# Kernel optimization log

Measured on AMD Instinct MI355X. Metric: run time of the kernel, lower is better.

## Reference

```python
import math
import jax, jax.numpy as jnp
import numpy as np

D_MODEL = 1024
D_HIDDEN = 4096
N_EXPERTS = 8
TOP_K = 2
CAPACITY_FACTOR = 1.25


def setup_inputs() -> dict:
    key = jax.random.key(0)
    ks = jax.random.split(key, 8)
    s = 0.02
    x = jax.random.normal(ks[0], (4, 2048, D_MODEL), dtype=jnp.float32)
    router_w = jax.random.normal(ks[1], (D_MODEL, N_EXPERTS), dtype=jnp.float32) * s
    router_b = jnp.zeros((N_EXPERTS,), dtype=jnp.float32)
    w1 = jax.random.normal(ks[2], (N_EXPERTS, D_MODEL, D_HIDDEN), dtype=jnp.float32) * s
    b1 = jnp.zeros((N_EXPERTS, D_HIDDEN), dtype=jnp.float32)
    w2 = jax.random.normal(ks[3], (N_EXPERTS, D_HIDDEN, D_MODEL), dtype=jnp.float32) * s
    b2 = jnp.zeros((N_EXPERTS, D_MODEL), dtype=jnp.float32)
    return {"x": x, "router_w": router_w, "router_b": router_b,
            "w1": w1, "b1": b1, "w2": w2, "b2": b2}


def reference(x, router_w, router_b, w1, b1, w2, b2):
    B, T, D = x.shape
    N = B * T
    E = N_EXPERTS
    capacity = max(1, math.ceil(N / E * CAPACITY_FACTOR))

    x_flat = x.reshape(N, D)
    # Router (torch casts input to float32 for router)
    logits = x_flat.astype(jnp.float32) @ router_w + router_b          # [N, E]
    gates = jax.nn.softmax(logits, axis=-1)                            # [N, E]

    _, topk_idx = jax.lax.top_k(gates, TOP_K)                          # [N, k]
    expert_mask = jax.nn.one_hot(topk_idx, E, dtype=jnp.int32).sum(1)  # [N, E]

    # Capacity masking via cumulative position per expert
    pos = jnp.cumsum(expert_mask, axis=0) - 1                          # [N, E]
    expert_mask = expert_mask * (pos < capacity)
    valid = expert_mask > 0                                            # [N, E] bool

    # Dispatch: scatter tokens into [E, capacity, D] buffers (invalid -> slot `capacity`)
    pos_c = jnp.where(valid, pos, capacity)                            # [N, E]
    e_idx = jnp.broadcast_to(jnp.arange(E), (N, E))
    dispatched = (x_flat[:, None, :] * valid[:, :, None].astype(x.dtype))
    buf = jnp.zeros((E, capacity + 1, D), x.dtype).at[
        e_idx.ravel(), pos_c.ravel()].add(dispatched.reshape(N * E, D))
    buf = buf[:, :capacity]                                            # [E, C, D]

    # Per-expert FFN as batched GEMMs (GELU exact, matching nn.GELU default)
    h = jax.nn.gelu(jnp.einsum('ecd,edh->ech', buf, w1) + b1[:, None, :],
                    approximate=False)
    out = jnp.einsum('ech,ehd->ecd', h, w2) + b2[:, None, :]           # [E, C, D]

    # Combine: gather each token's expert outputs, weight by raw softmax gate
    pos_g = jnp.minimum(pos_c, capacity - 1)
    gathered = out[e_idx, pos_g]                                       # [N, E, D]
    weights = (gates * valid).astype(x.dtype)                          # [N, E]
    y = jnp.einsum('ned,ne->nd', gathered, weights)
    return y.reshape(B, T, D)
```

## Files before the change

### kernel.cpp

```cpp
#include <hip/hip_runtime.h>
#include <math.h>

#define D_MODEL 1024
#define D_HIDDEN 4096
#define NEXP 8
#define NTOK 8192
#define CAP 1280

#define BM 128
#define BN 128
#define BK2 64

typedef __attribute__((ext_vector_type(8))) short short8x;
typedef __attribute__((ext_vector_type(4))) short short4x;
typedef __attribute__((ext_vector_type(4))) float float4x;

__device__ __forceinline__ short f2bf(float f) {
  unsigned u = __float_as_uint(f);
  unsigned r = (u + 0x7FFFu + ((u >> 16) & 1u)) >> 16;
  return (short)r;
}
__device__ __forceinline__ float bf2f(short s) {
  return __uint_as_float(((unsigned)(unsigned short)s) << 16);
}
__device__ __forceinline__ float gelu_fast(float v) {
  float u2 = v * (1.5957691216f + 0.0713548163f * v * v);
  return v / (1.0f + __expf(-u2));
}

#define GLDS16(g, l)                                                        \
  __builtin_amdgcn_global_load_lds(                                         \
      (const __attribute__((address_space(1))) void*)(g),                   \
      (__attribute__((address_space(3))) void*)(l), 16, 0, 0)

__global__ __launch_bounds__(256) void convert_x_kernel(
    const float* __restrict__ x, short* __restrict__ xbf) {
  size_t i = ((size_t)blockIdx.x * 256 + threadIdx.x) * 8;
  const float4* s = (const float4*)(x + i);
  float4 a = s[0], b = s[1];
  short8x o;
  o[0] = f2bf(a.x); o[1] = f2bf(a.y); o[2] = f2bf(a.z); o[3] = f2bf(a.w);
  o[4] = f2bf(b.x); o[5] = f2bf(b.y); o[6] = f2bf(b.z); o[7] = f2bf(b.w);
  *(short8x*)(xbf + i) = o;
}

__global__ __launch_bounds__(256) void transpose_kernel(
    const float* __restrict__ in, short* __restrict__ out, int K, int N) {
  __shared__ short tile[64][65];
  int n0 = blockIdx.x * 64, k0 = blockIdx.y * 64, e = blockIdx.z;
  int tid = threadIdx.x;
  int cr = tid >> 4;
  int cc = (tid & 15) * 4;
  const float* src = in + (size_t)e * K * N;
#pragma unroll
  for (int p = 0; p < 4; ++p) {
    int r = p * 16 + cr;
    float4 v = *(const float4*)(src + (size_t)(k0 + r) * N + n0 + cc);
    tile[r][cc] = f2bf(v.x); tile[r][cc + 1] = f2bf(v.y);
    tile[r][cc + 2] = f2bf(v.z); tile[r][cc + 3] = f2bf(v.w);
  }
  __syncthreads();
  short* dst = out + (size_t)e * N * K;
#pragma unroll
  for (int p = 0; p < 4; ++p) {
    int nr = p * 16 + cr;
    short4x s;
#pragma unroll
    for (int j = 0; j < 4; ++j) s[j] = tile[cc + j][nr];
    *(short4x*)(dst + (size_t)(n0 + nr) * K + k0 + cc) = s;
  }
}

__global__ __launch_bounds__(256) void router_kernel(
    const float* __restrict__ x, const float* __restrict__ rw,
    const float* __restrict__ rb, int2* __restrict__ tok_experts,
    float2* __restrict__ tok_gates) {
  int t = blockIdx.x * 4 + (threadIdx.x >> 6);
  int lane = threadIdx.x & 63;
  const float* xr = x + (size_t)t * D_MODEL;
  float acc[8];
#pragma unroll
  for (int e = 0; e < 8; ++e) acc[e] = 0.f;
#pragma unroll
  for (int kk = 0; kk < 16; ++kk) {
    int k = kk * 64 + lane;
    float xv = xr[k];
    const float4* wr = (const float4*)(rw + (size_t)k * 8);
    float4 w0 = wr[0], w1v = wr[1];
    acc[0] += xv * w0.x;  acc[1] += xv * w0.y;
    acc[2] += xv * w0.z;  acc[3] += xv * w0.w;
    acc[4] += xv * w1v.x; acc[5] += xv * w1v.y;
    acc[6] += xv * w1v.z; acc[7] += xv * w1v.w;
  }
#pragma unroll
  for (int off = 32; off > 0; off >>= 1) {
#pragma unroll
    for (int e = 0; e < 8; ++e) acc[e] += __shfl_xor(acc[e], off, 64);
  }
  if (lane == 0) {
    float lg[8];
#pragma unroll
    for (int e = 0; e < 8; ++e) lg[e] = acc[e] + rb[e];
    int e0 = 0;
#pragma unroll
    for (int e = 1; e < 8; ++e) if (lg[e] > lg[e0]) e0 = e;
    int e1 = (e0 == 0) ? 1 : 0;
#pragma unroll
    for (int e = 0; e < 8; ++e) if (e != e0 && lg[e] > lg[e1]) e1 = e;
    float mx = lg[e0];
    float s = 0.f;
#pragma unroll
    for (int e = 0; e < 8; ++e) s += expf(lg[e] - mx);
    float inv = 1.f / s;
    tok_experts[t] = make_int2(e0, e1);
    tok_gates[t] = make_float2(expf(lg[e0] - mx) * inv, expf(lg[e1] - mx) * inv);
  }
}

__global__ __launch_bounds__(1024) void scan_kernel(
    const int2* __restrict__ tok_experts, int* __restrict__ slot_token,
    int* __restrict__ token_rows) {
  int e = blockIdx.x;
  int tid = threadIdx.x;
  for (int i = tid; i < CAP; i += 1024) slot_token[e * CAP + i] = -1;
  __shared__ int wsum[16];
  __shared__ int running;
  if (tid == 0) running = 0;
  __syncthreads();
  int lane = tid & 63, wid = tid >> 6;
  unsigned long long lmask = (1ull << lane) - 1ull;
  for (int base = 0; base < NTOK; base += 1024) {
    int t = base + tid;
    int2 ee = tok_experts[t];
    int m = (ee.x == e || ee.y == e) ? 1 : 0;
    unsigned long long bal = __ballot(m);
    int prefix = __popcll(bal & lmask);
    if (lane == 0) wsum[wid] = (int)__popcll(bal);
    __syncthreads();
    if (tid == 0) {
      int s = running;
#pragma unroll
      for (int w = 0; w < 16; ++w) { int v = wsum[w]; wsum[w] = s; s += v; }
      running = s;
    }
    __syncthreads();
    if (m) {
      int pos = wsum[wid] + prefix;
      int which = (ee.x == e) ? 0 : 1;
      if (pos < CAP) {
        slot_token[e * CAP + pos] = t;
        token_rows[2 * t + which] = e * CAP + pos;
      } else {
        token_rows[2 * t + which] = -1;
      }
    }
    __syncthreads();
  }
}


__global__ __launch_bounds__(256) void gemm1_fast(
    const short* __restrict__ xbf, const short* __restrict__ w1t,
    const float* __restrict__ b1, const int* __restrict__ slot_token,
    short* __restrict__ h) {
  __shared__ short As[BM * BK2];
  __shared__ short Bs[BN * BK2];
  __shared__ int rowtok[BM];
  int e = blockIdx.z, rt = blockIdx.y, ct = blockIdx.x;
  int tid = threadIdx.x;
  if (tid < BM) {
    int t = slot_token[e * CAP + rt * BM + tid];
    rowtok[tid] = t < 0 ? 0 : t;
  }
  __syncthreads();
  int lane = tid & 63, w = tid >> 6;

  int srow = w * 8 + (lane >> 3);
  int slot = lane & 7;
  int cA = (slot - ((srow >> 1) & 7)) & 7;
  const char* agm[4];
  char* alds[4];
  char* blds[4];
#pragma unroll
  for (int p = 0; p < 4; ++p) {
    int r = p * 32 + srow;
    agm[p] = (const char*)(xbf + (size_t)rowtok[r] * D_MODEL) + cA * 16;
    alds[p] = (char*)As + (r * 8 + slot) * 16;
    blds[p] = (char*)Bs + (r * 8 + slot) * 16;
  }
  const char* bgm0 =
      (const char*)(w1t + ((size_t)e * D_HIDDEN + ct * BN + srow) * D_MODEL) + cA * 16;
  const size_t bstride = (size_t)32 * D_MODEL * 2;

  int l15 = lane & 15, q = lane >> 4;
  const char* A0 = (const char*)As + (w * 32 + l15) * 128;
  const char* B0 = (const char*)Bs + l15 * 128;
  int sw0 = (((q + (l15 >> 1)) & 7)) * 16;
  int sw1 = (((4 + q + (l15 >> 1)) & 7)) * 16;

  float4x acc[2][8];
#pragma unroll
  for (int i = 0; i < 2; ++i)
#pragma unroll
    for (int j = 0; j < 8; ++j) acc[i][j] = (float4x){0.f, 0.f, 0.f, 0.f};

  for (int k0 = 0; k0 < D_MODEL; k0 += BK2) {
    __syncthreads();
    int kb = k0 * 2;
#pragma unroll
    for (int p = 0; p < 4; ++p) GLDS16(agm[p] + kb, alds[p]);
#pragma unroll
    for (int p = 0; p < 4; ++p) GLDS16(bgm0 + p * bstride + kb, blds[p]);
    __syncthreads();
    short8x a00 = *(const short8x*)(A0 + sw0);
    short8x a10 = *(const short8x*)(A0 + 2048 + sw0);
    short8x a01 = *(const short8x*)(A0 + sw1);
    short8x a11 = *(const short8x*)(A0 + 2048 + sw1);
#pragma unroll
    for (int j = 0; j < 8; ++j) {
      short8x b0 = *(const short8x*)(B0 + j * 2048 + sw0);
      acc[0][j] = __builtin_amdgcn_mfma_f32_16x16x32_bf16(a00, b0, acc[0][j], 0, 0, 0);
      acc[1][j] = __builtin_amdgcn_mfma_f32_16x16x32_bf16(a10, b0, acc[1][j], 0, 0, 0);
      short8x b1v = *(const short8x*)(B0 + j * 2048 + sw1);
      acc[0][j] = __builtin_amdgcn_mfma_f32_16x16x32_bf16(a01, b1v, acc[0][j], 0, 0, 0);
      acc[1][j] = __builtin_amdgcn_mfma_f32_16x16x32_bf16(a11, b1v, acc[1][j], 0, 0, 0);
    }
  }
  int col0 = ct * BN;
  int rbase = q * 4;
#pragma unroll
  for (int i = 0; i < 2; ++i) {
#pragma unroll
    for (int j = 0; j < 8; ++j) {
      int col = col0 + j * 16 + l15;
      float bias = b1[e * D_HIDDEN + col];
#pragma unroll
      for (int r = 0; r < 4; ++r) {
        int grow = rt * BM + w * 32 + i * 16 + rbase + r;
        float v = gelu_fast(acc[i][j][r] + bias);
        h[(size_t)(e * CAP + grow) * D_HIDDEN + col] = f2bf(v);
      }
    }
  }
}

__global__ __launch_bounds__(256) void gemm2_fast(
    const short* __restrict__ h, const short* __restrict__ w2t,
    const float* __restrict__ b2, short* __restrict__ out2) {
  __shared__ short As[BM * BK2];
  __shared__ short Bs[BN * BK2];
  int e = blockIdx.z, rt = blockIdx.y, ct = blockIdx.x;
  int tid = threadIdx.x;
  int lane = tid & 63, w = tid >> 6;

  int srow = w * 8 + (lane >> 3);
  int slot = lane & 7;
  int cA = (slot - ((srow >> 1) & 7)) & 7;
  char* alds[4];
  char* blds[4];
#pragma unroll
  for (int p = 0; p < 4; ++p) {
    int r = p * 32 + srow;
    alds[p] = (char*)As + (r * 8 + slot) * 16;
    blds[p] = (char*)Bs + (r * 8 + slot) * 16;
  }
  const char* agm0 =
      (const char*)(h + (size_t)(e * CAP + rt * BM + srow) * D_HIDDEN) + cA * 16;
  const char* bgm0 =
      (const char*)(w2t + ((size_t)e * D_MODEL + ct * BN + srow) * D_HIDDEN) + cA * 16;
  const size_t astride = (size_t)32 * D_HIDDEN * 2;

  int l15 = lane & 15, q = lane >> 4;
  const char* A0 = (const char*)As + (w * 32 + l15) * 128;
  const char* B0 = (const char*)Bs + l15 * 128;
  int sw0 = (((q + (l15 >> 1)) & 7)) * 16;
  int sw1 = (((4 + q + (l15 >> 1)) & 7)) * 16;

  float4x acc[2][8];
#pragma unroll
  for (int i = 0; i < 2; ++i)
#pragma unroll
    for (int j = 0; j < 8; ++j) acc[i][j] = (float4x){0.f, 0.f, 0.f, 0.f};

  for (int k0 = 0; k0 < D_HIDDEN; k0 += BK2) {
    __syncthreads();
    int kb = k0 * 2;
#pragma unroll
    for (int p = 0; p < 4; ++p) GLDS16(agm0 + p * astride + kb, alds[p]);
#pragma unroll
    for (int p = 0; p < 4; ++p) GLDS16(bgm0 + p * astride + kb, blds[p]);
    __syncthreads();
    short8x a00 = *(const short8x*)(A0 + sw0);
    short8x a10 = *(const short8x*)(A0 + 2048 + sw0);
    short8x a01 = *(const short8x*)(A0 + sw1);
    short8x a11 = *(const short8x*)(A0 + 2048 + sw1);
#pragma unroll
    for (int j = 0; j < 8; ++j) {
      short8x b0 = *(const short8x*)(B0 + j * 2048 + sw0);
      acc[0][j] = __builtin_amdgcn_mfma_f32_16x16x32_bf16(a00, b0, acc[0][j], 0, 0, 0);
      acc[1][j] = __builtin_amdgcn_mfma_f32_16x16x32_bf16(a10, b0, acc[1][j], 0, 0, 0);
      short8x b1v = *(const short8x*)(B0 + j * 2048 + sw1);
      acc[0][j] = __builtin_amdgcn_mfma_f32_16x16x32_bf16(a01, b1v, acc[0][j], 0, 0, 0);
      acc[1][j] = __builtin_amdgcn_mfma_f32_16x16x32_bf16(a11, b1v, acc[1][j], 0, 0, 0);
    }
  }
  int col0 = ct * BN;
  int rbase = q * 4;
#pragma unroll
  for (int i = 0; i < 2; ++i) {
#pragma unroll
    for (int j = 0; j < 8; ++j) {
      int col = col0 + j * 16 + l15;
      float bias = b2[e * D_MODEL + col];
#pragma unroll
      for (int r = 0; r < 4; ++r) {
        int grow = rt * BM + w * 32 + i * 16 + rbase + r;
        float v = acc[i][j][r] + bias;
        out2[(size_t)(e * CAP + grow) * D_MODEL + col] = f2bf(v);
      }
    }
  }
}

__global__ __launch_bounds__(256) void combine_kernel(
    const int* __restrict__ token_rows, const float2* __restrict__ tok_gates,
    const short* __restrict__ out2, float* __restrict__ y) {
  int t = blockIdx.x;
  int r0 = token_rows[2 * t], r1 = token_rows[2 * t + 1];
  float2 g = tok_gates[t];
  int d = threadIdx.x * 4;
  float4 v; v.x = v.y = v.z = v.w = 0.f;
  if (r0 >= 0) {
    short4x a = *(const short4x*)(out2 + (size_t)r0 * D_MODEL + d);
    v.x += g.x * bf2f(a[0]); v.y += g.x * bf2f(a[1]);
    v.z += g.x * bf2f(a[2]); v.w += g.x * bf2f(a[3]);
  }
  if (r1 >= 0) {
    short4x a = *(const short4x*)(out2 + (size_t)r1 * D_MODEL + d);
    v.x += g.y * bf2f(a[0]); v.y += g.y * bf2f(a[1]);
    v.z += g.y * bf2f(a[2]); v.w += g.y * bf2f(a[3]);
  }
  *(float4*)(y + (size_t)t * D_MODEL + d) = v;
}

extern "C" void kernel_launch(void* const* d_in, const int* in_sizes, int n_in,
                              void* d_out, int out_size, void* d_ws, size_t ws_size,
                              hipStream_t stream) {
  const float* x  = (const float*)d_in[0];
  const float* rw = (const float*)d_in[1];
  const float* rb = (const float*)d_in[2];
  const float* w1 = (const float*)d_in[3];
  const float* b1 = (const float*)d_in[4];
  const float* w2 = (const float*)d_in[5];
  const float* b2 = (const float*)d_in[6];
  float* y = (float*)d_out;
  (void)in_sizes; (void)n_in; (void)out_size; (void)ws_size;

  char* p = (char*)d_ws;
  size_t off = 0;
  auto take = [&](size_t bytes) -> void* {
    void* r = p + off;
    off = (off + bytes + 255) & ~(size_t)255;
    return r;
  };
  int2*   tok_experts = (int2*)  take((size_t)NTOK * sizeof(int2));
  float2* tok_gates   = (float2*)take((size_t)NTOK * sizeof(float2));
  int*    slot_token  = (int*)   take((size_t)NEXP * CAP * sizeof(int));
  int*    token_rows  = (int*)   take((size_t)NTOK * 2 * sizeof(int));
  short*  xbf         = (short*) take((size_t)NTOK * D_MODEL * sizeof(short));
  short*  w1t         = (short*) take((size_t)NEXP * D_HIDDEN * D_MODEL * sizeof(short));
  short*  w2t         = (short*) take((size_t)NEXP * D_MODEL * D_HIDDEN * sizeof(short));
  short*  h           = (short*) take((size_t)NEXP * CAP * D_HIDDEN * sizeof(short));
  short*  out2        = (short*) take((size_t)NEXP * CAP * D_MODEL * sizeof(short));

  router_kernel<<<NTOK / 4, 256, 0, stream>>>(x, rw, rb, tok_experts, tok_gates);
  scan_kernel<<<NEXP, 1024, 0, stream>>>(tok_experts, slot_token, token_rows);
  convert_x_kernel<<<NTOK * D_MODEL / (256 * 8), 256, 0, stream>>>(x, xbf);
  transpose_kernel<<<dim3(D_HIDDEN / 64, D_MODEL / 64, NEXP), 256, 0, stream>>>(
      w1, w1t, D_MODEL, D_HIDDEN);
  transpose_kernel<<<dim3(D_MODEL / 64, D_HIDDEN / 64, NEXP), 256, 0, stream>>>(
      w2, w2t, D_HIDDEN, D_MODEL);
  gemm1_fast<<<dim3(D_HIDDEN / BN, CAP / BM, NEXP), 256, 0, stream>>>(
      xbf, w1t, b1, slot_token, h);
  gemm2_fast<<<dim3(D_MODEL / BN, CAP / BM, NEXP), 256, 0, stream>>>(
      h, w2t, b2, out2);
  combine_kernel<<<NTOK, 256, 0, stream>>>(token_rows, tok_gates, out2, y);
}
```

Measured before the change: 696.2 us.

## Split-K gemm2, shrink K tile, reorder block indices, repack transpose

Several changes at once. The GEMM K-tile drops from 64 to 32, which halves the LDS footprint and changes the swizzle. Block indices are flattened with the expert in the low bits so that concurrent blocks share weights. gemm2 is split along K into two halves, written to separate partial buffers (one reuses the w1t workspace), and summed in the combine kernel, which doubles gemm2's grid. The weight transpose now packs pairs of bf16 into 32-bit words via lane shuffles to widen its LDS and global stores. Risks are more barriers per K step and the extra partial-buffer traffic.

```diff
diff --git a/kernel.cpp b/kernel.cpp
--- a/kernel.cpp
+++ b/kernel.cpp
@@ -9,7 +9,9 @@
 
 #define BM 128
 #define BN 128
-#define BK2 64
+#define BK 32
+#define KSPLIT 2
+#define KHALF (D_HIDDEN / KSPLIT)
 
 typedef __attribute__((ext_vector_type(8))) short short8x;
 typedef __attribute__((ext_vector_type(4))) short short4x;
@@ -46,29 +48,44 @@
 
 __global__ __launch_bounds__(256) void transpose_kernel(
     const float* __restrict__ in, short* __restrict__ out, int K, int N) {
-  __shared__ short tile[64][65];
+  __shared__ unsigned tile[32 * 65];
   int n0 = blockIdx.x * 64, k0 = blockIdx.y * 64, e = blockIdx.z;
-  int tid = threadIdx.x;
-  int cr = tid >> 4;
-  int cc = (tid & 15) * 4;
-  const float* src = in + (size_t)e * K * N;
+  int t = threadIdx.x;
+  int rr = t >> 4;
+  int cc = (t & 15) * 4;
+  const float* src = in + (size_t)e * K * N + (size_t)(k0 + rr) * N + n0 + cc;
+  bool packer = (rr & 1) == 0;
+  int mb = rr >> 1;
 #pragma unroll
   for (int p = 0; p < 4; ++p) {
-    int r = p * 16 + cr;
-    float4 v = *(const float4*)(src + (size_t)(k0 + r) * N + n0 + cc);
-    tile[r][cc] = f2bf(v.x); tile[r][cc + 1] = f2bf(v.y);
-    tile[r][cc + 2] = f2bf(v.z); tile[r][cc + 3] = f2bf(v.w);
+    float4 v = *(const float4*)(src + (size_t)p * 16 * N);
+    float4 wv;
+    wv.x = __shfl_xor(v.x, 16, 64);
+    wv.y = __shfl_xor(v.y, 16, 64);
+    wv.z = __shfl_xor(v.z, 16, 64);
+    wv.w = __shfl_xor(v.w, 16, 64);
+    if (packer) {
+      int m = p * 8 + mb;
+      unsigned* tr = &tile[m * 65 + cc];
+      tr[0] = (unsigned)(unsigned short)f2bf(v.x) |
+              ((unsigned)(unsigned short)f2bf(wv.x) << 16);
+      tr[1] = (unsigned)(unsigned short)f2bf(v.y) |
+              ((unsigned)(unsigned short)f2bf(wv.y) << 16);
+      tr[2] = (unsigned)(unsigned short)f2bf(v.z) |
+              ((unsigned)(unsigned short)f2bf(wv.z) << 16);
+      tr[3] = (unsigned)(unsigned short)f2bf(v.w) |
+              ((unsigned)(unsigned short)f2bf(wv.w) << 16);
+    }
   }
   __syncthreads();
-  short* dst = out + (size_t)e * N * K;
-#pragma unroll
-  for (int p = 0; p < 4; ++p) {
-    int nr = p * 16 + cr;
-    short4x s;
-#pragma unroll
-    for (int j = 0; j < 4; ++j) s[j] = tile[cc + j][nr];
-    *(short4x*)(dst + (size_t)(n0 + nr) * K + k0 + cc) = s;
-  }
+  int n = t >> 2, q = t & 3;
+  const unsigned* col = &tile[q * 8 * 65 + n];
+  unsigned d[8];
+#pragma unroll
+  for (int j = 0; j < 8; ++j) d[j] = col[j * 65];
+  short* dst = out + (size_t)e * N * K + (size_t)(n0 + n) * K + k0 + q * 16;
+  ((uint4*)dst)[0] = make_uint4(d[0], d[1], d[2], d[3]);
+  ((uint4*)dst)[1] = make_uint4(d[4], d[5], d[6], d[7]);
 }
 
 __global__ __launch_bounds__(256) void router_kernel(
@@ -163,10 +180,11 @@
     const short* __restrict__ xbf, const short* __restrict__ w1t,
     const float* __restrict__ b1, const int* __restrict__ slot_token,
     short* __restrict__ h) {
-  __shared__ short As[BM * BK2];
-  __shared__ short Bs[BN * BK2];
+  __shared__ short As[BM * BK];
+  __shared__ short Bs[BN * BK];
   __shared__ int rowtok[BM];
-  int e = blockIdx.z, rt = blockIdx.y, ct = blockIdx.x;
+  int bx = blockIdx.x;
+  int e = bx & 7, ct = (bx >> 3) & 31, rt = bx >> 8;
   int tid = threadIdx.x;
   if (tid < BM) {
     int t = slot_token[e * CAP + rt * BM + tid];
@@ -175,28 +193,21 @@
   __syncthreads();
   int lane = tid & 63, w = tid >> 6;
 
-  int srow = w * 8 + (lane >> 3);
-  int slot = lane & 7;
-  int cA = (slot - ((srow >> 1) & 7)) & 7;
-  const char* agm[4];
-  char* alds[4];
-  char* blds[4];
-#pragma unroll
-  for (int p = 0; p < 4; ++p) {
-    int r = p * 32 + srow;
-    agm[p] = (const char*)(xbf + (size_t)rowtok[r] * D_MODEL) + cA * 16;
-    alds[p] = (char*)As + (r * 8 + slot) * 16;
-    blds[p] = (char*)Bs + (r * 8 + slot) * 16;
-  }
-  const char* bgm0 =
-      (const char*)(w1t + ((size_t)e * D_HIDDEN + ct * BN + srow) * D_MODEL) + cA * 16;
-  const size_t bstride = (size_t)32 * D_MODEL * 2;
-
+  const char* agm[2]; const char* bgm[2];
+  char* alds[2]; char* blds[2];
+#pragma unroll
+  for (int p = 0; p < 2; ++p) {
+    int r = w * 32 + p * 16 + (lane >> 2);
+    int c = ((lane & 3) - ((r >> 1) & 3)) & 3;
+    agm[p] = (const char*)(xbf + (size_t)rowtok[r] * D_MODEL + c * 8);
+    alds[p] = (char*)As + (w * 32 + p * 16) * 64 + lane * 16;
+    bgm[p] = (const char*)(w1t + ((size_t)e * D_HIDDEN + ct * BN + r) * D_MODEL + c * 8);
+    blds[p] = (char*)Bs + (w * 32 + p * 16) * 64 + lane * 16;
+  }
   int l15 = lane & 15, q = lane >> 4;
-  const char* A0 = (const char*)As + (w * 32 + l15) * 128;
-  const char* B0 = (const char*)Bs + l15 * 128;
-  int sw0 = (((q + (l15 >> 1)) & 7)) * 16;
-  int sw1 = (((4 + q + (l15 >> 1)) & 7)) * 16;
+  int swz = (q + ((l15 >> 1) & 3)) & 3;
+  const char* afb = (const char*)As + (w * 32 + l15) * 64 + swz * 16;
+  const char* bfb = (const char*)Bs + l15 * 64 + swz * 16;
 
   float4x acc[2][8];
 #pragma unroll
@@ -204,26 +215,21 @@
 #pragma unroll
     for (int j = 0; j < 8; ++j) acc[i][j] = (float4x){0.f, 0.f, 0.f, 0.f};
 
-  for (int k0 = 0; k0 < D_MODEL; k0 += BK2) {
+  for (int k0 = 0; k0 < D_MODEL; k0 += BK) {
     __syncthreads();
     int kb = k0 * 2;
-#pragma unroll
-    for (int p = 0; p < 4; ++p) GLDS16(agm[p] + kb, alds[p]);
-#pragma unroll
-    for (int p = 0; p < 4; ++p) GLDS16(bgm0 + p * bstride + kb, blds[p]);
-    __syncthreads();
-    short8x a00 = *(const short8x*)(A0 + sw0);
-    short8x a10 = *(const short8x*)(A0 + 2048 + sw0);
-    short8x a01 = *(const short8x*)(A0 + sw1);
-    short8x a11 = *(const short8x*)(A0 + 2048 + sw1);
+    GLDS16(agm[0] + kb, alds[0]);
+    GLDS16(agm[1] + kb, alds[1]);
+    GLDS16(bgm[0] + kb, blds[0]);
+    GLDS16(bgm[1] + kb, blds[1]);
+    __syncthreads();
+    short8x a0 = *(const short8x*)afb;
+    short8x a1 = *(const short8x*)(afb + 1024);
 #pragma unroll
     for (int j = 0; j < 8; ++j) {
-      short8x b0 = *(const short8x*)(B0 + j * 2048 + sw0);
-      acc[0][j] = __builtin_amdgcn_mfma_f32_16x16x32_bf16(a00, b0, acc[0][j], 0, 0, 0);
-      acc[1][j] = __builtin_amdgcn_mfma_f32_16x16x32_bf16(a10, b0, acc[1][j], 0, 0, 0);
-      short8x b1v = *(const short8x*)(B0 + j * 2048 + sw1);
-      acc[0][j] = __builtin_amdgcn_mfma_f32_16x16x32_bf16(a01, b1v, acc[0][j], 0, 0, 0);
-      acc[1][j] = __builtin_amdgcn_mfma_f32_16x16x32_bf16(a11, b1v, acc[1][j], 0, 0, 0);
+      short8x b = *(const short8x*)(bfb + j * 1024);
+      acc[0][j] = __builtin_amdgcn_mfma_f32_16x16x32_bf16(a0, b, acc[0][j], 0, 0, 0);
+      acc[1][j] = __builtin_amdgcn_mfma_f32_16x16x32_bf16(a1, b, acc[1][j], 0, 0, 0);
     }
   }
   int col0 = ct * BN;
@@ -246,35 +252,35 @@
 
 __global__ __launch_bounds__(256) void gemm2_fast(
     const short* __restrict__ h, const short* __restrict__ w2t,
-    const float* __restrict__ b2, short* __restrict__ out2) {
-  __shared__ short As[BM * BK2];
-  __shared__ short Bs[BN * BK2];
-  int e = blockIdx.z, rt = blockIdx.y, ct = blockIdx.x;
+    const float* __restrict__ b2, short* __restrict__ p0,
+    short* __restrict__ p1) {
+  __shared__ short As[BM * BK];
+  __shared__ short Bs[BN * BK];
+  int bx = blockIdx.x;
+  int e = bx & 7;
+  int rest = bx >> 3;
+  int ct = rest & 7;
+  int rg = rest >> 3;
+  int rt = rg >> 1, ks = rg & 1;
+  int koff = ks * KHALF;
   int tid = threadIdx.x;
   int lane = tid & 63, w = tid >> 6;
 
-  int srow = w * 8 + (lane >> 3);
-  int slot = lane & 7;
-  int cA = (slot - ((srow >> 1) & 7)) & 7;
-  char* alds[4];
-  char* blds[4];
-#pragma unroll
-  for (int p = 0; p < 4; ++p) {
-    int r = p * 32 + srow;
-    alds[p] = (char*)As + (r * 8 + slot) * 16;
-    blds[p] = (char*)Bs + (r * 8 + slot) * 16;
-  }
-  const char* agm0 =
-      (const char*)(h + (size_t)(e * CAP + rt * BM + srow) * D_HIDDEN) + cA * 16;
-  const char* bgm0 =
-      (const char*)(w2t + ((size_t)e * D_MODEL + ct * BN + srow) * D_HIDDEN) + cA * 16;
-  const size_t astride = (size_t)32 * D_HIDDEN * 2;
-
+  const char* agm[2]; const char* bgm[2];
+  char* alds[2]; char* blds[2];
+#pragma unroll
+  for (int p = 0; p < 2; ++p) {
+    int r = w * 32 + p * 16 + (lane >> 2);
+    int c = ((lane & 3) - ((r >> 1) & 3)) & 3;
+    agm[p] = (const char*)(h + (size_t)(e * CAP + rt * BM + r) * D_HIDDEN + koff + c * 8);
+    alds[p] = (char*)As + (w * 32 + p * 16) * 64 + lane * 16;
+    bgm[p] = (const char*)(w2t + ((size_t)e * D_MODEL + ct * BN + r) * D_HIDDEN + koff + c * 8);
+    blds[p] = (char*)Bs + (w * 32 + p * 16) * 64 + lane * 16;
+  }
   int l15 = lane & 15, q = lane >> 4;
-  const char* A0 = (const char*)As + (w * 32 + l15) * 128;
-  const char* B0 = (const char*)Bs + l15 * 128;
-  int sw0 = (((q + (l15 >> 1)) & 7)) * 16;
-  int sw1 = (((4 + q + (l15 >> 1)) & 7)) * 16;
+  int swz = (q + ((l15 >> 1) & 3)) & 3;
+  const char* afb = (const char*)As + (w * 32 + l15) * 64 + swz * 16;
+  const char* bfb = (const char*)Bs + l15 * 64 + swz * 16;
 
   float4x acc[2][8];
 #pragma unroll
@@ -282,28 +288,24 @@
 #pragma unroll
     for (int j = 0; j < 8; ++j) acc[i][j] = (float4x){0.f, 0.f, 0.f, 0.f};
 
-  for (int k0 = 0; k0 < D_HIDDEN; k0 += BK2) {
+  for (int k0 = 0; k0 < KHALF; k0 += BK) {
     __syncthreads();
     int kb = k0 * 2;
-#pragma unroll
-    for (int p = 0; p < 4; ++p) GLDS16(agm0 + p * astride + kb, alds[p]);
-#pragma unroll
-    for (int p = 0; p < 4; ++p) GLDS16(bgm0 + p * astride + kb, blds[p]);
-    __syncthreads();
-    short8x a00 = *(const short8x*)(A0 + sw0);
-    short8x a10 = *(const short8x*)(A0 + 2048 + sw0);
-    short8x a01 = *(const short8x*)(A0 + sw1);
-    short8x a11 = *(const short8x*)(A0 + 2048 + sw1);
+    GLDS16(agm[0] + kb, alds[0]);
+    GLDS16(agm[1] + kb, alds[1]);
+    GLDS16(bgm[0] + kb, blds[0]);
+    GLDS16(bgm[1] + kb, blds[1]);
+    __syncthreads();
+    short8x a0 = *(const short8x*)afb;
+    short8x a1 = *(const short8x*)(afb + 1024);
 #pragma unroll
     for (int j = 0; j < 8; ++j) {
-      short8x b0 = *(const short8x*)(B0 + j * 2048 + sw0);
-      acc[0][j] = __builtin_amdgcn_mfma_f32_16x16x32_bf16(a00, b0, acc[0][j], 0, 0, 0);
-      acc[1][j] = __builtin_amdgcn_mfma_f32_16x16x32_bf16(a10, b0, acc[1][j], 0, 0, 0);
-      short8x b1v = *(const short8x*)(B0 + j * 2048 + sw1);
-      acc[0][j] = __builtin_amdgcn_mfma_f32_16x16x32_bf16(a01, b1v, acc[0][j], 0, 0, 0);
-      acc[1][j] = __builtin_amdgcn_mfma_f32_16x16x32_bf16(a11, b1v, acc[1][j], 0, 0, 0);
-    }
-  }
+      short8x b = *(const short8x*)(bfb + j * 1024);
+      acc[0][j] = __builtin_amdgcn_mfma_f32_16x16x32_bf16(a0, b, acc[0][j], 0, 0, 0);
+      acc[1][j] = __builtin_amdgcn_mfma_f32_16x16x32_bf16(a1, b, acc[1][j], 0, 0, 0);
+    }
+  }
+  short* dst = ks == 0 ? p0 : p1;
   int col0 = ct * BN;
   int rbase = q * 4;
 #pragma unroll
@@ -311,12 +313,12 @@
 #pragma unroll
     for (int j = 0; j < 8; ++j) {
       int col = col0 + j * 16 + l15;
-      float bias = b2[e * D_MODEL + col];
+      float bias = (ks == 0) ? b2[e * D_MODEL + col] : 0.f;
 #pragma unroll
       for (int r = 0; r < 4; ++r) {
         int grow = rt * BM + w * 32 + i * 16 + rbase + r;
         float v = acc[i][j][r] + bias;
-        out2[(size_t)(e * CAP + grow) * D_MODEL + col] = f2bf(v);
+        dst[(size_t)(e * CAP + grow) * D_MODEL + col] = f2bf(v);
       }
     }
   }
@@ -324,21 +326,28 @@
 
 __global__ __launch_bounds__(256) void combine_kernel(
     const int* __restrict__ token_rows, const float2* __restrict__ tok_gates,
-    const short* __restrict__ out2, float* __restrict__ y) {
+    const short* __restrict__ p0, const short* __restrict__ p1,
+    float* __restrict__ y) {
   int t = blockIdx.x;
   int r0 = token_rows[2 * t], r1 = token_rows[2 * t + 1];
   float2 g = tok_gates[t];
   int d = threadIdx.x * 4;
   float4 v; v.x = v.y = v.z = v.w = 0.f;
   if (r0 >= 0) {
-    short4x a = *(const short4x*)(out2 + (size_t)r0 * D_MODEL + d);
-    v.x += g.x * bf2f(a[0]); v.y += g.x * bf2f(a[1]);
-    v.z += g.x * bf2f(a[2]); v.w += g.x * bf2f(a[3]);
+    short4x a = *(const short4x*)(p0 + (size_t)r0 * D_MODEL + d);
+    short4x b = *(const short4x*)(p1 + (size_t)r0 * D_MODEL + d);
+    v.x += g.x * (bf2f(a[0]) + bf2f(b[0]));
+    v.y += g.x * (bf2f(a[1]) + bf2f(b[1]));
+    v.z += g.x * (bf2f(a[2]) + bf2f(b[2]));
+    v.w += g.x * (bf2f(a[3]) + bf2f(b[3]));
   }
   if (r1 >= 0) {
-    short4x a = *(const short4x*)(out2 + (size_t)r1 * D_MODEL + d);
-    v.x += g.y * bf2f(a[0]); v.y += g.y * bf2f(a[1]);
-    v.z += g.y * bf2f(a[2]); v.w += g.y * bf2f(a[3]);
+    short4x a = *(const short4x*)(p0 + (size_t)r1 * D_MODEL + d);
+    short4x b = *(const short4x*)(p1 + (size_t)r1 * D_MODEL + d);
+    v.x += g.y * (bf2f(a[0]) + bf2f(b[0]));
+    v.y += g.y * (bf2f(a[1]) + bf2f(b[1]));
+    v.z += g.y * (bf2f(a[2]) + bf2f(b[2]));
+    v.w += g.y * (bf2f(a[3]) + bf2f(b[3]));
   }
   *(float4*)(y + (size_t)t * D_MODEL + d) = v;
 }
@@ -372,6 +381,8 @@
   short*  w2t         = (short*) take((size_t)NEXP * D_MODEL * D_HIDDEN * sizeof(short));
   short*  h           = (short*) take((size_t)NEXP * CAP * D_HIDDEN * sizeof(short));
   short*  out2        = (short*) take((size_t)NEXP * CAP * D_MODEL * sizeof(short));
+  short* part0 = out2;
+  short* part1 = w1t;
 
   router_kernel<<<NTOK / 4, 256, 0, stream>>>(x, rw, rb, tok_experts, tok_gates);
   scan_kernel<<<NEXP, 1024, 0, stream>>>(tok_experts, slot_token, token_rows);
@@ -380,9 +391,7 @@
       w1, w1t, D_MODEL, D_HIDDEN);
   transpose_kernel<<<dim3(D_MODEL / 64, D_HIDDEN / 64, NEXP), 256, 0, stream>>>(
       w2, w2t, D_HIDDEN, D_MODEL);
-  gemm1_fast<<<dim3(D_HIDDEN / BN, CAP / BM, NEXP), 256, 0, stream>>>(
-      xbf, w1t, b1, slot_token, h);
-  gemm2_fast<<<dim3(D_MODEL / BN, CAP / BM, NEXP), 256, 0, stream>>>(
-      h, w2t, b2, out2);
-  combine_kernel<<<NTOK, 256, 0, stream>>>(token_rows, tok_gates, out2, y);
-}
+  gemm1_fast<<<2560, 256, 0, stream>>>(xbf, w1t, b1, slot_token, h);
+  gemm2_fast<<<1280, 256, 0, stream>>>(h, w2t, b2, part0, part1);
+  combine_kernel<<<NTOK, 256, 0, stream>>>(token_rows, tok_gates, part0, part1, y);
+}
```

Measured after the change: 619.9 us. 11.0% less time.
